# Kernel tuning notes

Hardware: AMD Instinct MI355X
Metric: run time of the kernel (lower is better)

Reference implementation:

```python
import jax, jax.numpy as jnp
import numpy as np

N_NODES = 80_000
D_IN = 128
D_HID = 128
D_EMB = 64
N_EDGES = 2_560_000
NUM_PEAKS = 40_000
N_TF = 128
N_GENE = 8_000
MLP_HID = 128
N_OUT = 2


def setup_inputs() -> dict:
    key = jax.random.key(0)
    ks = jax.random.split(key, 8)
    x = jax.random.normal(ks[0], (N_NODES, D_IN), jnp.float32)
    edge_index = jax.random.randint(ks[1], (2, N_EDGES), 0, N_NODES)
    tf_index_list = jax.random.randint(ks[2], (N_TF,), 0, N_NODES - NUM_PEAKS)
    gene_index_list = jax.random.randint(ks[3], (N_GENE,), 0, N_NODES - NUM_PEAKS)
    s = lambda k, shp, fan: jax.random.normal(k, shp, jnp.float32) * np.float32(1.0 / np.sqrt(fan))
    W1 = s(ks[4], (D_IN, D_HID), D_IN)
    b1 = jnp.zeros((D_HID,), jnp.float32)
    W2 = s(ks[5], (D_HID, D_EMB), D_HID)
    b2 = jnp.zeros((D_EMB,), jnp.float32)
    Wm1 = s(ks[6], (2 * D_EMB, MLP_HID), 2 * D_EMB)
    bm1 = jnp.zeros((MLP_HID,), jnp.float32)
    Wm2 = s(ks[7], (MLP_HID, N_OUT), MLP_HID)
    bm2 = jnp.zeros((N_OUT,), jnp.float32)
    return dict(x=x, W1=W1, b1=b1, W2=W2, b2=b2, Wm1=Wm1, bm1=bm1, Wm2=Wm2, bm2=bm2,
                edge_index=edge_index, num=NUM_PEAKS,
                tf_index_list=tf_index_list, gene_index_list=gene_index_list)


def _gcn_agg(h, src, dst, n):
    # mean aggregation of neighbor features: agg[i] = mean_{(j->i) in E} h[j]
    deg = jax.ops.segment_sum(jnp.ones((src.shape[0],), h.dtype), dst, num_segments=n)
    agg = jax.ops.segment_sum(h[src], dst, num_segments=n)
    return agg / jnp.maximum(deg, 1.0)[:, None]


def reference(x, W1, b1, W2, b2, Wm1, bm1, Wm2, bm2,
              edge_index, num, tf_index_list, gene_index_list):
    src, dst = edge_index[0], edge_index[1]
    n = x.shape[0]
    # 2-layer GCN (mean aggregation) -> node embeddings [N, D_EMB]
    h = jax.nn.relu(_gcn_agg(x, src, dst, n) @ W1 + b1)
    emb = _gcn_agg(h, src, dst, n) @ W2 + b2
    # split_tensor(emb, num): pX = emb[:num] (unused), gX = emb[num:]
    gX = emb[num:]
    tf_emb = gX[tf_index_list]      # [T, d]
    g_emb = gX[gene_index_list]     # [G, d]
    T, d = tf_emb.shape
    G = g_emb.shape[0]
    # vectorized equivalent of the nested (tf, gene) concat loop; row order = tf*G + g
    combined = jnp.concatenate([
        jnp.broadcast_to(tf_emb[:, None, :], (T, G, d)),
        jnp.broadcast_to(g_emb[None, :, :], (T, G, d)),
    ], axis=-1).reshape(T * G, 2 * d)
    hid = jax.nn.relu(combined @ Wm1 + bm1)
    out = hid @ Wm2 + bm2
    return jax.nn.softmax(out, axis=-1)
```

## Files before the change

kernel.cpp:

```cpp
#include <hip/hip_runtime.h>
#include <math.h>

#define DIM 128
#define DEMB 64
#define CHUNK 8192


__device__ __forceinline__ unsigned pack_bf16x2(float a, float b) {
    unsigned ua = __float_as_uint(a);
    unsigned ub = __float_as_uint(b);
    ua = (ua + 0x7fffu + ((ua >> 16) & 1u)) >> 16;
    ub = (ub + 0x7fffu + ((ub >> 16) & 1u)) & 0xffff0000u;
    return ua | ub;
}
__device__ __forceinline__ float lo_bf16(unsigned v) { return __uint_as_float(v << 16); }
__device__ __forceinline__ float hi_bf16(unsigned v) { return __uint_as_float(v & 0xffff0000u); }


__global__ __launch_bounds__(256) void convert_kernel(const float* __restrict__ in,
                                                      unsigned* __restrict__ out, int n2) {
    int i = blockIdx.x * 256 + threadIdx.x;
    int stride = gridDim.x * 256;
    for (; i < n2; i += stride) {
        float2 v = reinterpret_cast<const float2*>(in)[i];
        out[i] = pack_bf16x2(v.x, v.y);
    }
}


__global__ __launch_bounds__(256) void bucket_count(const int* __restrict__ dst,
                                                    int* __restrict__ bcnt,
                                                    int n_edges, int nbuck) {
    __shared__ int h[384];
    for (int i = threadIdx.x; i < nbuck; i += 256) h[i] = 0;
    __syncthreads();
    int i = blockIdx.x * 256 + threadIdx.x;
    int stride = gridDim.x * 256;
    for (; i < n_edges; i += stride) atomicAdd(&h[dst[i] >> 8], 1);
    __syncthreads();
    for (int i2 = threadIdx.x; i2 < nbuck; i2 += 256)
        if (h[i2]) atomicAdd(&bcnt[i2], h[i2]);
}

__global__ __launch_bounds__(512) void bucket_scan(const int* __restrict__ bcnt,
                                                   int* __restrict__ bstart,
                                                   int* __restrict__ bcursor,
                                                   int nbuck, int n_edges) {
    __shared__ int sm[512];
    int tid = threadIdx.x;
    int v = (tid < nbuck) ? bcnt[tid] : 0;
    sm[tid] = v;
    __syncthreads();
    for (int off = 1; off < 512; off <<= 1) {
        int t = (tid >= off) ? sm[tid - off] : 0;
        __syncthreads();
        if (tid >= off) sm[tid] += t;
        __syncthreads();
    }
    if (tid < nbuck) {
        int e = sm[tid] - v;
        bstart[tid] = e;
        bcursor[tid] = e;
    }
    if (tid == 0) bstart[nbuck] = n_edges;
}

__global__ __launch_bounds__(256) void bucket_scatter(const int* __restrict__ src,
                                                      const int* __restrict__ dst,
                                                      int* __restrict__ bcursor,
                                                      unsigned* __restrict__ binned,
                                                      int n_edges, int nbuck) {
    __shared__ unsigned stage[CHUNK];
    __shared__ unsigned short bkt[CHUNK];
    __shared__ int cnt[384], off[384], gbase[384], cur[384];
    __shared__ int sc[256];
    __shared__ int tot0;
    int tid = threadIdx.x;
    int e0 = blockIdx.x * CHUNK;
    int ne = min(CHUNK, n_edges - e0);
    for (int i = tid; i < nbuck; i += 256) cnt[i] = 0;
    __syncthreads();
    for (int j = tid; j < ne; j += 256) atomicAdd(&cnt[dst[e0 + j] >> 8], 1);
    __syncthreads();
    {
        int v0 = (tid < nbuck) ? cnt[tid] : 0;
        sc[tid] = v0;
        __syncthreads();
        for (int o = 1; o < 256; o <<= 1) {
            int t = (tid >= o) ? sc[tid - o] : 0;
            __syncthreads();
            sc[tid] += t;
            __syncthreads();
        }
        if (tid < nbuck) off[tid] = sc[tid] - v0;
        if (tid == 255) tot0 = sc[255];
        __syncthreads();
        int i1 = 256 + tid;
        int v1 = (i1 < nbuck) ? cnt[i1] : 0;
        sc[tid] = v1;
        __syncthreads();
        for (int o = 1; o < 256; o <<= 1) {
            int t = (tid >= o) ? sc[tid - o] : 0;
            __syncthreads();
            sc[tid] += t;
            __syncthreads();
        }
        if (i1 < nbuck) off[i1] = tot0 + sc[tid] - v1;
        __syncthreads();
    }
    for (int b = tid; b < nbuck; b += 256) {
        cur[b] = off[b];
        gbase[b] = cnt[b] ? atomicAdd(&bcursor[b], cnt[b]) : 0;
    }
    __syncthreads();
    for (int j = tid; j < ne; j += 256) {
        int d = dst[e0 + j];
        int s = src[e0 + j];
        int b = d >> 8;
        int p = atomicAdd(&cur[b], 1);
        stage[p] = ((unsigned)s << 8) | (unsigned)(d & 255);
        bkt[p] = (unsigned short)b;
    }
    __syncthreads();
    for (int j = tid; j < ne; j += 256) {
        int b = bkt[j];
        binned[gbase[b] + (j - off[b])] = stage[j];
    }
}

__global__ __launch_bounds__(256) void bucket_csr(const unsigned* __restrict__ binned,
                                                  const int* __restrict__ bstart,
                                                  int* __restrict__ counts,
                                                  int* __restrict__ rowstart,
                                                  int* __restrict__ ssorted,
                                                  int n_nodes) {
    __shared__ int sm[256], cur[256];
    __shared__ int cntv[256];
    int b = blockIdx.x;
    int bs = bstart[b], be = bstart[b + 1];
    int node0 = b << 8;
    int tid = threadIdx.x;
    cntv[tid] = 0;
    __syncthreads();
    for (int j = bs + tid; j < be; j += 256) atomicAdd(&cntv[binned[j] & 255u], 1);
    __syncthreads();
    int v = cntv[tid];
    sm[tid] = v;
    __syncthreads();
    for (int off = 1; off < 256; off <<= 1) {
        int t = (tid >= off) ? sm[tid - off] : 0;
        __syncthreads();
        if (tid >= off) sm[tid] += t;
        __syncthreads();
    }
    int excl = sm[tid] - v;
    int node = node0 + tid;
    if (node < n_nodes) {
        counts[node] = v;
        rowstart[node] = bs + excl;
    }
    cur[tid] = excl;
    __syncthreads();
    for (int j = bs + tid; j < be; j += 256) {
        unsigned e = binned[j];
        int p = atomicAdd(&cur[(int)(e & 255u)], 1);
        ssorted[bs + p] = (int)(e >> 8);
    }
}


__global__ __launch_bounds__(256) void agg_kernel(const unsigned* __restrict__ xh,
                                                  const int* __restrict__ rowstart,
                                                  const int* __restrict__ counts,
                                                  const int* __restrict__ ssorted,
                                                  unsigned* __restrict__ Ah, int n_nodes) {
    int wave = (blockIdx.x * 256 + threadIdx.x) >> 6;
    int lane = threadIdx.x & 63;
    if (wave >= n_nodes) return;
    int base = rowstart[wave];
    int deg = counts[wave];
    const unsigned* xp = xh + lane;
    float ax = 0.f, ay = 0.f;
    int j = 0;
    for (; j + 8 <= deg; j += 8) {
        int s0 = ssorted[base + j];
        int s1 = ssorted[base + j + 1];
        int s2 = ssorted[base + j + 2];
        int s3 = ssorted[base + j + 3];
        int s4 = ssorted[base + j + 4];
        int s5 = ssorted[base + j + 5];
        int s6 = ssorted[base + j + 6];
        int s7 = ssorted[base + j + 7];
        unsigned v0 = xp[(size_t)s0 * 64];
        unsigned v1 = xp[(size_t)s1 * 64];
        unsigned v2 = xp[(size_t)s2 * 64];
        unsigned v3 = xp[(size_t)s3 * 64];
        unsigned v4 = xp[(size_t)s4 * 64];
        unsigned v5 = xp[(size_t)s5 * 64];
        unsigned v6 = xp[(size_t)s6 * 64];
        unsigned v7 = xp[(size_t)s7 * 64];
        ax += ((lo_bf16(v0) + lo_bf16(v1)) + (lo_bf16(v2) + lo_bf16(v3))) +
              ((lo_bf16(v4) + lo_bf16(v5)) + (lo_bf16(v6) + lo_bf16(v7)));
        ay += ((hi_bf16(v0) + hi_bf16(v1)) + (hi_bf16(v2) + hi_bf16(v3))) +
              ((hi_bf16(v4) + hi_bf16(v5)) + (hi_bf16(v6) + hi_bf16(v7)));
    }
    for (; j < deg; j++) {
        int s = ssorted[base + j];
        unsigned v = xp[(size_t)s * 64];
        ax += lo_bf16(v);
        ay += hi_bf16(v);
    }
    float inv = 1.f / fmaxf((float)deg, 1.f);
    Ah[(size_t)wave * 64 + lane] = pack_bf16x2(ax * inv, ay * inv);
}


__global__ __launch_bounds__(256) void gemm1_kernel(const unsigned* __restrict__ Ah,
                                                    const float* __restrict__ W1,
                                                    const float* __restrict__ b1,
                                                    unsigned* __restrict__ Hh, int n_rows) {
    __shared__ float W1s[DIM * DIM];
    __shared__ unsigned As[32 * 64];
    int tid = threadIdx.x;
    for (int i = 0; i < 16; i++) {
        int idx = (i * 256 + tid) * 4;
        *reinterpret_cast<float4*>(&W1s[idx]) = *reinterpret_cast<const float4*>(&W1[idx]);
    }
    int r0 = blockIdx.x * 32;
    for (int i = 0; i < 2; i++) {
        int idx = (i * 256 + tid) * 4;
        int gr = r0 + (idx >> 6);
        uint4 vv = {0, 0, 0, 0};
        if (gr < n_rows) vv = *reinterpret_cast<const uint4*>(&Ah[(size_t)r0 * 64 + idx]);
        *reinterpret_cast<uint4*>(&As[idx]) = vv;
    }
    __syncthreads();
    int tx = tid & 31, ty = tid >> 5;
    float4 b = *reinterpret_cast<const float4*>(&b1[tx * 4]);
    float acc[4][4];
#pragma unroll
    for (int i = 0; i < 4; i++) {
        acc[i][0] = b.x; acc[i][1] = b.y; acc[i][2] = b.z; acc[i][3] = b.w;
    }
#pragma unroll 8
    for (int kc = 0; kc < 32; kc++) {
        int k = kc * 4;
        float4 w0 = *reinterpret_cast<const float4*>(&W1s[(k + 0) * DIM + tx * 4]);
        float4 w1 = *reinterpret_cast<const float4*>(&W1s[(k + 1) * DIM + tx * 4]);
        float4 w2 = *reinterpret_cast<const float4*>(&W1s[(k + 2) * DIM + tx * 4]);
        float4 w3 = *reinterpret_cast<const float4*>(&W1s[(k + 3) * DIM + tx * 4]);
#pragma unroll
        for (int i = 0; i < 4; i++) {
            uint2 av = *reinterpret_cast<const uint2*>(&As[(ty * 4 + i) * 64 + kc * 2]);
            float a0 = lo_bf16(av.x), a1 = hi_bf16(av.x);
            float a2 = lo_bf16(av.y), a3 = hi_bf16(av.y);
            acc[i][0] += a0 * w0.x; acc[i][1] += a0 * w0.y; acc[i][2] += a0 * w0.z; acc[i][3] += a0 * w0.w;
            acc[i][0] += a1 * w1.x; acc[i][1] += a1 * w1.y; acc[i][2] += a1 * w1.z; acc[i][3] += a1 * w1.w;
            acc[i][0] += a2 * w2.x; acc[i][1] += a2 * w2.y; acc[i][2] += a2 * w2.z; acc[i][3] += a2 * w2.w;
            acc[i][0] += a3 * w3.x; acc[i][1] += a3 * w3.y; acc[i][2] += a3 * w3.z; acc[i][3] += a3 * w3.w;
        }
    }
#pragma unroll
    for (int i = 0; i < 4; i++) {
        int r = r0 + ty * 4 + i;
        if (r < n_rows) {
            float o0 = fmaxf(acc[i][0], 0.f);
            float o1 = fmaxf(acc[i][1], 0.f);
            float o2 = fmaxf(acc[i][2], 0.f);
            float o3 = fmaxf(acc[i][3], 0.f);
            uint2 pk = {pack_bf16x2(o0, o1), pack_bf16x2(o2, o3)};
            *reinterpret_cast<uint2*>(&Hh[(size_t)r * 64 + tx * 2]) = pk;
        }
    }
}


__global__ __launch_bounds__(256) void target_kernel(const unsigned* __restrict__ Hh,
                                                     const float* __restrict__ W2,
                                                     const float* __restrict__ b2,
                                                     const int* __restrict__ rowstart,
                                                     const int* __restrict__ counts,
                                                     const int* __restrict__ ssorted,
                                                     const int* __restrict__ dnum,
                                                     const int* __restrict__ tf_idx,
                                                     const int* __restrict__ gene_idx,
                                                     float* __restrict__ emb, int T, int ntar) {
    __shared__ float W2s[DIM * DEMB];
    __shared__ float aggS[4][DIM];
    int tid = threadIdx.x;
    for (int i = 0; i < 8; i++) {
        int idx = (i * 256 + tid) * 4;
        *reinterpret_cast<float4*>(&W2s[idx]) = *reinterpret_cast<const float4*>(&W2[idx]);
    }
    int wv = tid >> 6, lane = tid & 63;
    int i = blockIdx.x * 4 + wv;
    int num = dnum[0];
    if (i < ntar) {
        int idx = (i < T) ? tf_idx[i] : gene_idx[i - T];
        int node = num + idx;
        int base = rowstart[node];
        int deg = counts[node];
        const unsigned* hp = Hh + lane;
        float ax = 0.f, ay = 0.f;
        int j = 0;
        for (; j + 4 <= deg; j += 4) {
            int s0 = ssorted[base + j];
            int s1 = ssorted[base + j + 1];
            int s2 = ssorted[base + j + 2];
            int s3 = ssorted[base + j + 3];
            unsigned v0 = hp[(size_t)s0 * 64];
            unsigned v1 = hp[(size_t)s1 * 64];
            unsigned v2 = hp[(size_t)s2 * 64];
            unsigned v3 = hp[(size_t)s3 * 64];
            ax += (lo_bf16(v0) + lo_bf16(v1)) + (lo_bf16(v2) + lo_bf16(v3));
            ay += (hi_bf16(v0) + hi_bf16(v1)) + (hi_bf16(v2) + hi_bf16(v3));
        }
        for (; j < deg; j++) {
            int s = ssorted[base + j];
            unsigned v = hp[(size_t)s * 64];
            ax += lo_bf16(v);
            ay += hi_bf16(v);
        }
        float inv = 1.f / fmaxf((float)deg, 1.f);
        float2 st = {ax * inv, ay * inv};
        *reinterpret_cast<float2*>(&aggS[wv][2 * lane]) = st;
    }
    __syncthreads();
    if (i < ntar) {
        float e = b2[lane];
#pragma unroll 4
        for (int k = 0; k < DIM; k++) e += aggS[wv][k] * W2s[k * DEMB + lane];
        emb[(size_t)i * DEMB + lane] = e;
    }
}


__global__ __launch_bounds__(128) void ab_kernel(const float* __restrict__ emb,
                                                 const float* __restrict__ Wm1,
                                                 const float* __restrict__ bm1,
                                                 float* __restrict__ AB, int T, int ntar) {
    int i = blockIdx.x;
    int j = threadIdx.x;
    if (i >= ntar) return;
    const float* e = emb + (size_t)i * DEMB;
    int base = (i < T) ? 0 : DEMB;
    float acc = (i < T) ? bm1[j] : 0.f;
#pragma unroll 4
    for (int k = 0; k < DEMB; k++) acc += e[k] * Wm1[(size_t)(base + k) * DIM + j];
    AB[(size_t)i * DIM + j] = acc;
}


__global__ __launch_bounds__(256) void final_kernel(const float* __restrict__ AB,
                                                    const float* __restrict__ Wm2,
                                                    const float* __restrict__ bm2,
                                                    float* __restrict__ out, int T, int G) {
    __shared__ float tfAs[8 * DIM];
    __shared__ float wd[DIM];
    int tid = threadIdx.x;
    int t0 = blockIdx.y * 8;
    int g0 = blockIdx.x * 256;
    {
        int idx = tid * 4;
        int t = t0 + (idx >> 7);
        float4 v = {0, 0, 0, 0};
        if (t < T) v = *reinterpret_cast<const float4*>(&AB[(size_t)t0 * DIM + idx]);
        *reinterpret_cast<float4*>(&tfAs[idx]) = v;
    }
    if (tid < DIM) wd[tid] = Wm2[tid * 2] - Wm2[tid * 2 + 1];
    __syncthreads();
    int g = g0 + tid;
    int gc = min(g, G - 1);
    const float4* gp = reinterpret_cast<const float4*>(AB + (size_t)(T + gc) * DIM);
    float acc[8];
#pragma unroll
    for (int t = 0; t < 8; t++) acc[t] = 0.f;
    for (int kc = 0; kc < 16; kc++) {
        float4 ga = gp[kc * 2];
        float4 gb = gp[kc * 2 + 1];
        float4 wa = *reinterpret_cast<const float4*>(&wd[kc * 8]);
        float4 wb = *reinterpret_cast<const float4*>(&wd[kc * 8 + 4]);
#pragma unroll
        for (int t = 0; t < 8; t++) {
            const float4 ta = *reinterpret_cast<const float4*>(&tfAs[t * DIM + kc * 8]);
            const float4 tb = *reinterpret_cast<const float4*>(&tfAs[t * DIM + kc * 8 + 4]);
            acc[t] += fmaxf(ta.x + ga.x, 0.f) * wa.x;
            acc[t] += fmaxf(ta.y + ga.y, 0.f) * wa.y;
            acc[t] += fmaxf(ta.z + ga.z, 0.f) * wa.z;
            acc[t] += fmaxf(ta.w + ga.w, 0.f) * wa.w;
            acc[t] += fmaxf(tb.x + gb.x, 0.f) * wb.x;
            acc[t] += fmaxf(tb.y + gb.y, 0.f) * wb.y;
            acc[t] += fmaxf(tb.z + gb.z, 0.f) * wb.z;
            acc[t] += fmaxf(tb.w + gb.w, 0.f) * wb.w;
        }
    }
    if (g < G) {
        float bd = bm2[0] - bm2[1];
#pragma unroll
        for (int t = 0; t < 8; t++) {
            if (t0 + t < T) {
                float d = acc[t] + bd;
                float p0 = 1.f / (1.f + __expf(-d));
                float2 r = {p0, 1.f - p0};
                *reinterpret_cast<float2*>(&out[((size_t)(t0 + t) * G + g) * 2]) = r;
            }
        }
    }
}


extern "C" void kernel_launch(void* const* d_in, const int* in_sizes, int n_in,
                              void* d_out, int out_size, void* d_ws, size_t ws_size,
                              hipStream_t stream) {
    const float* x    = (const float*)d_in[0];
    const float* W1   = (const float*)d_in[1];
    const float* b1   = (const float*)d_in[2];
    const float* W2   = (const float*)d_in[3];
    const float* b2   = (const float*)d_in[4];
    const float* Wm1  = (const float*)d_in[5];
    const float* bm1  = (const float*)d_in[6];
    const float* Wm2  = (const float*)d_in[7];
    const float* bm2  = (const float*)d_in[8];
    const int* ei     = (const int*)d_in[9];
    const int* dnum   = (const int*)d_in[10];
    const int* tfidx  = (const int*)d_in[11];
    const int* geidx  = (const int*)d_in[12];
    float* out = (float*)d_out;

    int n_nodes = in_sizes[0] / DIM;
    int n_edges = in_sizes[9] / 2;
    int T = in_sizes[11];
    int G = in_sizes[12];
    int ntar = T + G;
    int nbuck = (n_nodes + 255) >> 8;
    const int* srcp = ei;
    const int* dstp = ei + n_edges;

    char* w = (char*)d_ws;
    size_t o = 0;
    auto alloc = [&](size_t bytes) {
        void* p = w + o;
        o += (bytes + 255) & ~(size_t)255;
        return p;
    };
    unsigned* xh   = (unsigned*)alloc((size_t)n_nodes * 64 * 4);
    unsigned* Hh   = (unsigned*)alloc((size_t)n_nodes * 64 * 4);
    unsigned* Ah   = (unsigned*)alloc((size_t)n_nodes * 64 * 4);
    int* ssorted   = (int*)alloc((size_t)n_edges * 4);
    int* counts    = (int*)alloc((size_t)n_nodes * 4);
    int* rowstart  = (int*)alloc((size_t)n_nodes * 4);
    int* bcnt      = (int*)alloc(2048);
    int* bstart    = (int*)alloc(2048);
    int* bcursor   = (int*)alloc(2048);
    unsigned* binned = Hh;
    float* emb = (float*)Ah;
    float* AB  = (float*)Ah + (4u * 1024u * 1024u / 4u);

    hipMemsetAsync(bcnt, 0, (size_t)nbuck * 4, stream);

    convert_kernel<<<2048, 256, 0, stream>>>(x, xh, n_nodes * 64);
    bucket_count<<<1024, 256, 0, stream>>>(dstp, bcnt, n_edges, nbuck);
    bucket_scan<<<1, 512, 0, stream>>>(bcnt, bstart, bcursor, nbuck, n_edges);
    bucket_scatter<<<(n_edges + CHUNK - 1) / CHUNK, 256, 0, stream>>>(srcp, dstp, bcursor,
                                                                      binned, n_edges, nbuck);
    bucket_csr<<<nbuck, 256, 0, stream>>>(binned, bstart, counts, rowstart, ssorted, n_nodes);

    agg_kernel<<<(n_nodes + 3) / 4, 256, 0, stream>>>(xh, rowstart, counts, ssorted, Ah, n_nodes);
    gemm1_kernel<<<(n_nodes + 31) / 32, 256, 0, stream>>>(Ah, W1, b1, Hh, n_nodes);
    target_kernel<<<(ntar + 3) / 4, 256, 0, stream>>>(Hh, W2, b2, rowstart, counts, ssorted,
                                                      dnum, tfidx, geidx, emb, T, ntar);
    ab_kernel<<<ntar, 128, 0, stream>>>(emb, Wm1, bm1, AB, T, ntar);
    final_kernel<<<dim3((G + 255) / 256, (T + 7) / 8), 256, 0, stream>>>(AB, Wm2, bm2, out, T, G);
}
```

Before: 411.6 us.

## Use bf16 MFMA for first GCN GEMM and sort CSR neighbors by source

Replaces the scalar FP32 gemm1 with a bf16 MFMA 16x16x32 kernel that reads a pre-transposed, bf16-packed W1 from padded shared memory. The goal is to cut the ALU cost of the 80k x 128 x 128 layer-1 GEMM. Separately, bucket_csr now builds a 4096-bin histogram keyed by destination and the high bits of the source, so each node's neighbor list is roughly ordered by source index. That ordering should give the gather in agg and target kernels better cache locality. The cost is a larger shared histogram, an extra weight-prep launch, and W1 rounded to bf16.

```diff
diff --git a/kernel.cpp b/kernel.cpp
--- a/kernel.cpp
+++ b/kernel.cpp
@@ -4,6 +4,9 @@
 #define DIM 128
 #define DEMB 64
 #define CHUNK 8192
+
+typedef __attribute__((ext_vector_type(8))) short bf16x8;
+typedef __attribute__((ext_vector_type(4))) float f32x4;
 
 
 __device__ __forceinline__ unsigned pack_bf16x2(float a, float b) {
@@ -25,6 +28,17 @@
         float2 v = reinterpret_cast<const float2*>(in)[i];
         out[i] = pack_bf16x2(v.x, v.y);
     }
+}
+
+
+__global__ __launch_bounds__(256) void prep_w1t(const float* __restrict__ W1,
+                                                unsigned* __restrict__ W1t) {
+    int i = blockIdx.x * 256 + threadIdx.x;
+    if (i >= 128 * 64) return;
+    int n = i >> 6, k2 = i & 63;
+    float a = W1[(size_t)(2 * k2) * DIM + n];
+    float b = W1[(size_t)(2 * k2 + 1) * DIM + n];
+    W1t[i] = pack_bf16x2(a, b);
 }
 
 
@@ -134,36 +148,51 @@
                                                   int* __restrict__ rowstart,
                                                   int* __restrict__ ssorted,
                                                   int n_nodes) {
-    __shared__ int sm[256], cur[256];
-    __shared__ int cntv[256];
+    __shared__ int hist[4096];
+    __shared__ int psum[256];
     int b = blockIdx.x;
     int bs = bstart[b], be = bstart[b + 1];
     int node0 = b << 8;
     int tid = threadIdx.x;
-    cntv[tid] = 0;
-    __syncthreads();
-    for (int j = bs + tid; j < be; j += 256) atomicAdd(&cntv[binned[j] & 255u], 1);
-    __syncthreads();
-    int v = cntv[tid];
-    sm[tid] = v;
-    __syncthreads();
-    for (int off = 1; off < 256; off <<= 1) {
-        int t = (tid >= off) ? sm[tid - off] : 0;
-        __syncthreads();
-        if (tid >= off) sm[tid] += t;
-        __syncthreads();
-    }
-    int excl = sm[tid] - v;
+    for (int i = tid; i < 4096; i += 256) hist[i] = 0;
+    __syncthreads();
+    for (int j = bs + tid; j < be; j += 256) {
+        unsigned e = binned[j];
+        int key = (int)((e & 255u) << 4) | (int)((e >> 8) >> 13);
+        atomicAdd(&hist[key], 1);
+    }
+    __syncthreads();
+    int loc[16];
+    int s = 0;
+#pragma unroll
+    for (int k = 0; k < 16; k++) {
+        loc[k] = s;
+        s += hist[tid * 16 + k];
+    }
+    psum[tid] = s;
+    __syncthreads();
+    int v = psum[tid];
+    int acc = v;
+    for (int o = 1; o < 256; o <<= 1) {
+        int t = (tid >= o) ? psum[tid - o] : 0;
+        __syncthreads();
+        psum[tid] += t;
+        __syncthreads();
+    }
+    int excl = psum[tid] - v;
+    (void)acc;
+#pragma unroll
+    for (int k = 0; k < 16; k++) hist[tid * 16 + k] = excl + loc[k];
     int node = node0 + tid;
     if (node < n_nodes) {
-        counts[node] = v;
+        counts[node] = s;
         rowstart[node] = bs + excl;
     }
-    cur[tid] = excl;
     __syncthreads();
     for (int j = bs + tid; j < be; j += 256) {
         unsigned e = binned[j];
-        int p = atomicAdd(&cur[(int)(e & 255u)], 1);
+        int key = (int)((e & 255u) << 4) | (int)((e >> 8) >> 13);
+        int p = atomicAdd(&hist[key], 1);
         ssorted[bs + p] = (int)(e >> 8);
     }
 }
@@ -215,61 +244,54 @@
 }
 
 
-__global__ __launch_bounds__(256) void gemm1_kernel(const unsigned* __restrict__ Ah,
-                                                    const float* __restrict__ W1,
-                                                    const float* __restrict__ b1,
-                                                    unsigned* __restrict__ Hh, int n_rows) {
-    __shared__ float W1s[DIM * DIM];
-    __shared__ unsigned As[32 * 64];
-    int tid = threadIdx.x;
-    for (int i = 0; i < 16; i++) {
-        int idx = (i * 256 + tid) * 4;
-        *reinterpret_cast<float4*>(&W1s[idx]) = *reinterpret_cast<const float4*>(&W1[idx]);
-    }
-    int r0 = blockIdx.x * 32;
-    for (int i = 0; i < 2; i++) {
-        int idx = (i * 256 + tid) * 4;
-        int gr = r0 + (idx >> 6);
-        uint4 vv = {0, 0, 0, 0};
-        if (gr < n_rows) vv = *reinterpret_cast<const uint4*>(&Ah[(size_t)r0 * 64 + idx]);
-        *reinterpret_cast<uint4*>(&As[idx]) = vv;
-    }
-    __syncthreads();
-    int tx = tid & 31, ty = tid >> 5;
-    float4 b = *reinterpret_cast<const float4*>(&b1[tx * 4]);
-    float acc[4][4];
-#pragma unroll
-    for (int i = 0; i < 4; i++) {
-        acc[i][0] = b.x; acc[i][1] = b.y; acc[i][2] = b.z; acc[i][3] = b.w;
-    }
-#pragma unroll 8
-    for (int kc = 0; kc < 32; kc++) {
-        int k = kc * 4;
-        float4 w0 = *reinterpret_cast<const float4*>(&W1s[(k + 0) * DIM + tx * 4]);
-        float4 w1 = *reinterpret_cast<const float4*>(&W1s[(k + 1) * DIM + tx * 4]);
-        float4 w2 = *reinterpret_cast<const float4*>(&W1s[(k + 2) * DIM + tx * 4]);
-        float4 w3 = *reinterpret_cast<const float4*>(&W1s[(k + 3) * DIM + tx * 4]);
-#pragma unroll
-        for (int i = 0; i < 4; i++) {
-            uint2 av = *reinterpret_cast<const uint2*>(&As[(ty * 4 + i) * 64 + kc * 2]);
-            float a0 = lo_bf16(av.x), a1 = hi_bf16(av.x);
-            float a2 = lo_bf16(av.y), a3 = hi_bf16(av.y);
-            acc[i][0] += a0 * w0.x; acc[i][1] += a0 * w0.y; acc[i][2] += a0 * w0.z; acc[i][3] += a0 * w0.w;
-            acc[i][0] += a1 * w1.x; acc[i][1] += a1 * w1.y; acc[i][2] += a1 * w1.z; acc[i][3] += a1 * w1.w;
-            acc[i][0] += a2 * w2.x; acc[i][1] += a2 * w2.y; acc[i][2] += a2 * w2.z; acc[i][3] += a2 * w2.w;
-            acc[i][0] += a3 * w3.x; acc[i][1] += a3 * w3.y; acc[i][2] += a3 * w3.z; acc[i][3] += a3 * w3.w;
-        }
-    }
-#pragma unroll
-    for (int i = 0; i < 4; i++) {
-        int r = r0 + ty * 4 + i;
-        if (r < n_rows) {
-            float o0 = fmaxf(acc[i][0], 0.f);
-            float o1 = fmaxf(acc[i][1], 0.f);
-            float o2 = fmaxf(acc[i][2], 0.f);
-            float o3 = fmaxf(acc[i][3], 0.f);
-            uint2 pk = {pack_bf16x2(o0, o1), pack_bf16x2(o2, o3)};
-            *reinterpret_cast<uint2*>(&Hh[(size_t)r * 64 + tx * 2]) = pk;
+__global__ __launch_bounds__(256) void gemm1_mfma(const unsigned* __restrict__ Ah,
+                                                  const unsigned* __restrict__ W1t,
+                                                  const float* __restrict__ b1,
+                                                  unsigned* __restrict__ Hh, int n_rows) {
+    __shared__ unsigned Wt[128 * 68];
+    int tid = threadIdx.x;
+#pragma unroll
+    for (int i = 0; i < 32; i++) {
+        int idx = i * 256 + tid;
+        Wt[(idx >> 6) * 68 + (idx & 63)] = W1t[idx];
+    }
+    __syncthreads();
+    int wv = tid >> 6, l = tid & 63;
+    int r0w = blockIdx.x * 64 + wv * 16;
+    int arow = r0w + (l & 15);
+    int arowc = min(arow, n_rows - 1);
+    int kgrp = l >> 4;
+    const bf16x8* ap = reinterpret_cast<const bf16x8*>(Ah + (size_t)arowc * 64);
+    bf16x8 afrag[4];
+#pragma unroll
+    for (int s = 0; s < 4; s++) afrag[s] = ap[s * 4 + kgrp];
+
+    f32x4 acc[8];
+#pragma unroll
+    for (int nt = 0; nt < 8; nt++) {
+        float bias = b1[nt * 16 + (l & 15)];
+        acc[nt] = {bias, bias, bias, bias};
+    }
+#pragma unroll
+    for (int s = 0; s < 4; s++) {
+#pragma unroll
+        for (int nt = 0; nt < 8; nt++) {
+            bf16x8 bfrag = *reinterpret_cast<const bf16x8*>(
+                &Wt[(nt * 16 + (l & 15)) * 68 + s * 16 + kgrp * 4]);
+            acc[nt] = __builtin_amdgcn_mfma_f32_16x16x32_bf16(afrag[s], bfrag, acc[nt], 0, 0, 0);
+        }
+    }
+    bool even = (l & 1) == 0;
+#pragma unroll
+    for (int nt = 0; nt < 8; nt++) {
+#pragma unroll
+        for (int j = 0; j < 4; j++) {
+            float v = fmaxf(acc[nt][j], 0.f);
+            float vp = __shfl_xor(v, 1);
+            int r = r0w + ((l >> 4) << 2) + j;
+            if (even && r < n_rows) {
+                Hh[(size_t)r * 64 + nt * 8 + ((l & 15) >> 1)] = pack_bf16x2(v, vp);
+            }
         }
     }
 }
@@ -449,6 +471,7 @@
     int* ssorted   = (int*)alloc((size_t)n_edges * 4);
     int* counts    = (int*)alloc((size_t)n_nodes * 4);
     int* rowstart  = (int*)alloc((size_t)n_nodes * 4);
+    unsigned* W1t  = (unsigned*)alloc(128 * 64 * 4);
     int* bcnt      = (int*)alloc(2048);
     int* bstart    = (int*)alloc(2048);
     int* bcursor   = (int*)alloc(2048);
@@ -459,6 +482,7 @@
     hipMemsetAsync(bcnt, 0, (size_t)nbuck * 4, stream);
 
     convert_kernel<<<2048, 256, 0, stream>>>(x, xh, n_nodes * 64);
+    prep_w1t<<<32, 256, 0, stream>>>(W1, W1t);
     bucket_count<<<1024, 256, 0, stream>>>(dstp, bcnt, n_edges, nbuck);
     bucket_scan<<<1, 512, 0, stream>>>(bcnt, bstart, bcursor, nbuck, n_edges);
     bucket_scatter<<<(n_edges + CHUNK - 1) / CHUNK, 256, 0, stream>>>(srcp, dstp, bcursor,
@@ -466,7 +490,7 @@
     bucket_csr<<<nbuck, 256, 0, stream>>>(binned, bstart, counts, rowstart, ssorted, n_nodes);
 
     agg_kernel<<<(n_nodes + 3) / 4, 256, 0, stream>>>(xh, rowstart, counts, ssorted, Ah, n_nodes);
-    gemm1_kernel<<<(n_nodes + 31) / 32, 256, 0, stream>>>(Ah, W1, b1, Hh, n_nodes);
+    gemm1_mfma<<<(n_nodes + 63) / 64, 256, 0, stream>>>(Ah, W1t, b1, Hh, n_nodes);
     target_kernel<<<(ntar + 3) / 4, 256, 0, stream>>>(Hh, W2, b2, rowstart, counts, ssorted,
                                                       dnum, tfidx, geidx, emb, T, ntar);
     ab_kernel<<<ntar, 128, 0, stream>>>(emb, Wm1, bm1, AB, T, ntar);
```

Result: faster. 354.4 us (-13.9%).
